# Kernel tuning notes

Hardware: AMD Instinct MI355X
Metric: run time of the kernel (lower is better)

Reference implementation:

```python
import jax, jax.numpy as jnp
import numpy as np

B, L, D_MODEL = 2, 2048, 1024
D_INNER = 2 * D_MODEL          # expand * d_model
D_STATE = 16
D_CONV = 4
DT_RANK = (D_INNER + 15) // 16  # ceil(d_inner/16) = 128


def setup_inputs() -> dict:
    key = jax.random.key(0)
    ks = jax.random.split(key, 9)
    s = 0.02
    x = jax.random.normal(ks[0], (B, L, D_MODEL), jnp.float32)
    in_proj_w = jax.random.normal(ks[1], (2 * D_INNER, D_MODEL), jnp.float32) * s
    conv_w = jax.random.normal(ks[2], (D_INNER, 1, D_CONV), jnp.float32) * s  # depthwise, OIH
    conv_b = jax.random.normal(ks[3], (D_INNER,), jnp.float32) * s
    x_proj_w = jax.random.normal(ks[4], (DT_RANK + 2 * D_STATE, D_INNER), jnp.float32) * s
    dt_proj_w = jax.random.uniform(ks[5], (D_INNER, DT_RANK), jnp.float32, -0.1, 0.1)
    # dt bias: inverse-softplus of dt in [dt_min, dt_max]
    dt = jnp.exp(jax.random.uniform(ks[6], (D_INNER,), jnp.float32)
                 * (np.log(0.1) - np.log(0.001)) + np.log(0.001))
    dt = jnp.clip(dt, 1e-4, None)
    dt_proj_b = dt + jnp.log(-jnp.expm1(-dt))
    A_log = jnp.log(jnp.tile(jnp.arange(1, D_STATE + 1, dtype=jnp.float32), (D_INNER, 1)))
    D = jnp.ones((D_INNER,), jnp.float32)
    out_proj_w = jax.random.normal(ks[7], (D_MODEL, D_INNER), jnp.float32) * s
    return {"x": x, "in_proj_w": in_proj_w, "conv_w": conv_w, "conv_b": conv_b,
            "x_proj_w": x_proj_w, "dt_proj_w": dt_proj_w, "dt_proj_b": dt_proj_b,
            "A_log": A_log, "D": D, "out_proj_w": out_proj_w}


def _s6_forward(x, in_proj_w, conv_w, conv_b, x_proj_w, dt_proj_w, dt_proj_b,
                A_log, D, out_proj_w):
    b, l, _ = x.shape
    d_inner, n_state = A_log.shape
    dt_rank = dt_proj_w.shape[1]
    d_conv = conv_w.shape[-1]

    xz = x @ in_proj_w.T                          # [b, l, 2*d_inner]
    xb, z = jnp.split(xz, 2, axis=-1)

    # causal depthwise conv1d: pad left by d_conv-1, truncate to l
    xc = jnp.swapaxes(xb, 1, 2)                   # [b, d_inner, l]
    xc = jax.lax.conv_general_dilated(
        xc, conv_w, window_strides=(1,), padding=[(d_conv - 1, 0)],
        dimension_numbers=("NCH", "OIH", "NCH"), feature_group_count=d_inner)
    xc = xc + conv_b[None, :, None]
    u = jax.nn.silu(jnp.swapaxes(xc, 1, 2))       # [b, l, d_inner]

    x_dbl = u @ x_proj_w.T                        # [b, l, dt_rank + 2*n_state]
    dt_in, Bs, Cs = jnp.split(x_dbl, [dt_rank, dt_rank + n_state], axis=-1)
    dt = jax.nn.softplus(dt_in @ dt_proj_w.T + dt_proj_b)  # [b, l, d_inner]

    A = -jnp.exp(A_log)                           # [d_inner, n_state]

    def step(h, inp):
        u_t, dt_t, B_t, C_t = inp                 # [b,d], [b,d], [b,n], [b,n]
        dA = jnp.exp(dt_t[:, :, None] * A)        # [b, d, n]
        h = dA * h + (dt_t * u_t)[:, :, None] * B_t[:, None, :]
        y_t = jnp.einsum("bdn,bn->bd", h, C_t)
        return h, y_t

    h0 = jnp.zeros((b, d_inner, n_state), u.dtype)
    xs = (jnp.swapaxes(u, 0, 1), jnp.swapaxes(dt, 0, 1),
          jnp.swapaxes(Bs, 0, 1), jnp.swapaxes(Cs, 0, 1))
    _, ys = jax.lax.scan(step, h0, xs)            # ys: [l, b, d_inner]
    y = jnp.swapaxes(ys, 0, 1) + u * D
    y = y * jax.nn.silu(z)
    return y @ out_proj_w.T                       # [b, l, d_model]


def reference(x, in_proj_w, conv_w, conv_b, x_proj_w, dt_proj_w, dt_proj_b,
              A_log, D, out_proj_w):
    return _s6_forward(x, in_proj_w, conv_w, conv_b, x_proj_w, dt_proj_w,
                       dt_proj_b, A_log, D, out_proj_w)
```

## Files before the change

kernel.cpp:

```cpp
#include <hip/hip_runtime.h>
#include <hip/hip_bf16.h>
#include <math.h>


#define B_ 2
#define L_ 2048
#define DM_ 1024
#define DI_ 2048
#define NS_ 16
#define DTR_ 128
#define XPN_ 160
#define XPP_ 192
#define CH_ 64
#define CL_ 32
#define NCH_ 4096
#define SK_ 8

typedef __attribute__((ext_vector_type(8))) short short8;
typedef __attribute__((ext_vector_type(4))) float f32x4;

__device__ inline unsigned short bfbits(float f) {
    __hip_bfloat16 h = __float2bfloat16(f);
    return *reinterpret_cast<unsigned short*>(&h);
}

__device__ inline void gload16(const void* g, void* l) {
    __builtin_amdgcn_global_load_lds(
        (__attribute__((address_space(1))) const void*)g,
        (__attribute__((address_space(3))) void*)l, 16, 0, 0);
}

__global__ __launch_bounds__(256) void cast_pair(
    const float* __restrict__ s0, unsigned short* __restrict__ d0,
    const float* __restrict__ s1, unsigned short* __restrict__ d1, int nper)
{
    int i = (blockIdx.x * 256 + threadIdx.x) * 4;
    const float* s = s0;
    unsigned short* d = d0;
    if (i >= nper) { s = s1; d = d1; i -= nper; }
    float4 v = *(const float4*)(s + i);
    *(ushort4*)(d + i) = make_ushort4(bfbits(v.x), bfbits(v.y), bfbits(v.z), bfbits(v.w));
}

__global__ __launch_bounds__(256) void cast_flat(
    const float* __restrict__ s, unsigned short* __restrict__ o, int n)
{
    int i = (blockIdx.x * 256 + threadIdx.x) * 4;
    if (i >= n) return;
    float4 v = *(const float4*)(s + i);
    *(ushort4*)(o + i) = make_ushort4(bfbits(v.x), bfbits(v.y), bfbits(v.z), bfbits(v.w));
}

__global__ __launch_bounds__(256) void cast_w(
    const float* __restrict__ xp, unsigned short* __restrict__ WXP,
    const float* __restrict__ dtp, unsigned short* __restrict__ DTP)
{
    int i = (blockIdx.x * 256 + threadIdx.x) * 4;
    const int NW = XPP_ * DI_;
    if (i < NW) {
        int row = i >> 11;
        ushort4 o = make_ushort4(0, 0, 0, 0);
        if (row < XPN_) {
            float4 v = *(const float4*)(xp + i);
            o = make_ushort4(bfbits(v.x), bfbits(v.y), bfbits(v.z), bfbits(v.w));
        }
        *(ushort4*)(WXP + i) = o;
    } else {
        int j = i - NW;
        float4 v = *(const float4*)(dtp + j);
        *(ushort4*)(DTP + j) = make_ushort4(bfbits(v.x), bfbits(v.y), bfbits(v.z), bfbits(v.w));
    }
}

#define GBAR() do { __builtin_amdgcn_s_barrier(); __builtin_amdgcn_sched_barrier(0); } while (0)
#define GWLG() do { asm volatile("s_waitcnt lgkmcnt(0)" ::: "memory"); __builtin_amdgcn_sched_barrier(0); } while (0)
#define GWVM(N) do { asm volatile("s_waitcnt vmcnt(" #N ")" ::: "memory"); __builtin_amdgcn_sched_barrier(0); } while (0)

#define RDA(LA, SWZ, AR) do { _Pragma("unroll") \
    for (int i_ = 0; i_ < 8; ++i_) \
        AR[i_] = *(const short8*)((LA) + aBase + i_ * 2048 + (SWZ)); } while (0)
#define RDB(LB, SWZ, BR) do { _Pragma("unroll") \
    for (int n_ = 0; n_ < 4; ++n_) \
        BR[n_] = *(const short8*)((LB) + bBase + n_ * 2048 + (SWZ)); } while (0)

#define CLUSTER(AR, BR, NF0) do { \
    __builtin_amdgcn_s_setprio(1); \
    _Pragma("unroll") \
    for (int i_ = 0; i_ < 8; ++i_) { \
        acc[i_][NF0]     = __builtin_amdgcn_mfma_f32_16x16x32_bf16(AR[i_], BR[NF0],     acc[i_][NF0],     0, 0, 0); \
        acc[i_][NF0 + 1] = __builtin_amdgcn_mfma_f32_16x16x32_bf16(AR[i_], BR[NF0 + 1], acc[i_][NF0 + 1], 0, 0, 0); \
    } \
    __builtin_amdgcn_s_setprio(0); } while (0)

#define STAGE_A(KT, H, LA) do { \
    const char* gs_ = pA + (long)((H) * 128) * lda2 + (KT) * 128; \
    gload16(gs_ + aoffA,              (LA) + (H) * 16384 + ldsw); \
    gload16(gs_ + aoffA + 64 * (long)lda2, (LA) + (H) * 16384 + 8192 + ldsw); } while (0)
#define STAGE_B(KT, H, LB) do { \
    const char* gs_ = pB + (long)((H) * 128) * ldb2 + (KT) * 128; \
    gload16(gs_ + aoffB,              (LB) + (H) * 16384 + ldsw); \
    gload16(gs_ + aoffB + 64 * (long)ldb2, (LB) + (H) * 16384 + 8192 + ldsw); } while (0)

__global__ __launch_bounds__(512, 2) void gemm_256(
    const unsigned short* __restrict__ A, int lda,
    const unsigned short* __restrict__ B, int ldb,
    float* __restrict__ C, int ldc, int K)
{
    __shared__ __align__(16) char smem[131072];
    char* const L0A = smem;
    char* const L0B = smem + 32768;
    char* const L1A = smem + 65536;
    char* const L1B = smem + 98304;

    const int tid = threadIdx.x;
    const int lane = tid & 63, wave = tid >> 6;
    const int wr = wave >> 2, wc = wave & 3;
    const int m = lane & 15, g = lane >> 4;
    const int row0 = blockIdx.y * 256, col0 = blockIdx.x * 256;

    const int aBase = (wr * 128 + m) * 128;
    const int bBase = (wc * 64 + m) * 128;
    const int swz0 = (g ^ (m & 7)) << 4;
    const int swz1 = ((4 + g) ^ (m & 7)) << 4;

    const int lda2 = lda * 2, ldb2 = ldb * 2;
    const int rowq = tid >> 3;
    const int cswz = ((tid & 7) ^ (rowq & 7)) << 4;
    const long aoffA = (long)rowq * lda2 + cswz;
    const long aoffB = (long)rowq * ldb2 + cswz;
    const char* const pA = (const char*)(A + (long)row0 * lda);
    const char* const pB = (const char*)(B + (long)col0 * ldb);
    const int ldsw = wave << 10;

    f32x4 acc[8][4];
    const f32x4 zero = {0.f, 0.f, 0.f, 0.f};
#pragma unroll
    for (int i = 0; i < 8; ++i)
#pragma unroll
        for (int j = 0; j < 4; ++j) acc[i][j] = zero;

    short8 a0[8], a1[8], b0[4], b1[4];
    const int NT = K >> 6;

    STAGE_B(0, 0, L0B); STAGE_B(0, 1, L0B);
    STAGE_A(0, 0, L0A); STAGE_A(0, 1, L0A);
    STAGE_B(1, 0, L1B); STAGE_B(1, 1, L1B);
    STAGE_A(1, 0, L1A);
    GWVM(6); GBAR();

    for (int t = 0; t < NT - 2; t += 2) {
        RDA(L0A, swz0, a0); RDB(L0B, swz0, b0); RDB(L0B, swz1, b1);
        STAGE_A(t + 1, 1, L1A);
        GBAR(); GWLG();
        CLUSTER(a0, b0, 0);
        GBAR();
        RDA(L0A, swz1, a1);
        STAGE_B(t + 2, 0, L0B);
        GBAR(); GWLG();
        CLUSTER(a0, b0, 2);
        GBAR();
        STAGE_B(t + 2, 1, L0B);
        GBAR();
        CLUSTER(a1, b1, 0);
        GBAR();
        STAGE_A(t + 2, 0, L0A);
        GWVM(6); GBAR();
        CLUSTER(a1, b1, 2);
        GBAR();
        RDA(L1A, swz0, a0); RDB(L1B, swz0, b0); RDB(L1B, swz1, b1);
        STAGE_A(t + 2, 1, L0A);
        GBAR(); GWLG();
        CLUSTER(a0, b0, 0);
        GBAR();
        RDA(L1A, swz1, a1);
        STAGE_B(t + 3, 0, L1B);
        GBAR(); GWLG();
        CLUSTER(a0, b0, 2);
        GBAR();
        STAGE_B(t + 3, 1, L1B);
        GBAR();
        CLUSTER(a1, b1, 0);
        GBAR();
        STAGE_A(t + 3, 0, L1A);
        GWVM(6); GBAR();
        CLUSTER(a1, b1, 2);
        GBAR();
    }

    RDA(L0A, swz0, a0); RDB(L0B, swz0, b0); RDB(L0B, swz1, b1);
    STAGE_A(NT - 1, 1, L1A);
    GBAR(); GWLG();
    CLUSTER(a0, b0, 0);
    GBAR();
    RDA(L0A, swz1, a1);
    GBAR(); GWLG();
    CLUSTER(a0, b0, 2);
    GBAR();
    CLUSTER(a1, b1, 0);
    GBAR();
    GWVM(0); GBAR();
    CLUSTER(a1, b1, 2);
    GBAR();
    RDA(L1A, swz0, a0); RDB(L1B, swz0, b0); RDB(L1B, swz1, b1);
    GWLG();
    CLUSTER(a0, b0, 0);
    RDA(L1A, swz1, a1);
    GWLG();
    CLUSTER(a0, b0, 2);
    CLUSTER(a1, b1, 0);
    CLUSTER(a1, b1, 2);

    const int cr = g << 2;
#pragma unroll
    for (int i = 0; i < 8; ++i) {
        const long gr = row0 + wr * 128 + i * 16 + cr;
#pragma unroll
        for (int nf = 0; nf < 4; ++nf) {
            const int gc = col0 + wc * 64 + nf * 16 + m;
#pragma unroll
            for (int r = 0; r < 4; ++r)
                C[(gr + r) * (long)ldc + gc] = acc[i][nf][r];
        }
    }
}

__global__ __launch_bounds__(256, 2) void gemm_h64(
    const unsigned short* __restrict__ A, int lda,
    const unsigned short* __restrict__ B, int ldb,
    float* __restrict__ C, int ldc, int K)
{
    __shared__ unsigned short sA[128][32];
    __shared__ unsigned short sB[64][32];
    const int tid = threadIdx.x;
    const int lane = tid & 63, wave = tid >> 6;
    const int orig = blockIdx.y * 16 + blockIdx.x;
    const int wgid = (orig & 7) * 64 + (orig >> 3);
    const int row0 = (wgid >> 4) << 7;
    const int col0 = (wgid & 15) << 6;
    const int wr = wave >> 1, wc = wave & 1;
    const int m = lane & 15;
    const int ko = (lane >> 4) << 3;

    f32x4 acc[4][2];
    const f32x4 zero = {0.f, 0.f, 0.f, 0.f};
#pragma unroll
    for (int i = 0; i < 4; ++i)
#pragma unroll
        for (int j = 0; j < 2; ++j) acc[i][j] = zero;

    for (int k0 = 0; k0 < K; k0 += 32) {
#pragma unroll
        for (int c = 0; c < 2; ++c) {
            int idx = tid + (c << 8);
            int r = idx >> 2;
            int col8 = (idx & 3) << 3;
            char* la = (char*)sA + (((c << 8) + (wave << 6)) << 4);
            gload16(A + (long)(row0 + r) * lda + k0 + col8, la);
        }
        {
            int r = tid >> 2;
            int col8 = (tid & 3) << 3;
            char* lb = (char*)sB + ((wave << 6) << 4);
            gload16(B + (long)(col0 + r) * ldb + k0 + col8, lb);
        }
        __syncthreads();

        short8 af[4];
#pragma unroll
        for (int i = 0; i < 4; ++i)
            af[i] = *(const short8*)&sA[(wr << 6) + i * 16 + m][ko];
#pragma unroll
        for (int j = 0; j < 2; ++j) {
            short8 bf = *(const short8*)&sB[(wc << 5) + j * 16 + m][ko];
#pragma unroll
            for (int i = 0; i < 4; ++i)
                acc[i][j] = __builtin_amdgcn_mfma_f32_16x16x32_bf16(af[i], bf, acc[i][j], 0, 0, 0);
        }
        __syncthreads();
    }

    const int cr = (lane >> 4) << 2;
#pragma unroll
    for (int i = 0; i < 4; ++i) {
#pragma unroll
        for (int j = 0; j < 2; ++j) {
            int gr = row0 + (wr << 6) + i * 16 + cr;
            int gc = col0 + (wc << 5) + j * 16 + m;
#pragma unroll
            for (int r = 0; r < 4; ++r)
                C[(long)(gr + r) * ldc + gc] = acc[i][j][r];
        }
    }
}

enum { WE_NONE = 0, WE_SOFTPLUS = 1 };

template <int EPI>
__global__ __launch_bounds__(256) void gemm_w64(
    const unsigned short* __restrict__ A, int lda,
    const unsigned short* __restrict__ B, int ldb,
    float* __restrict__ C, int ldc,
    const float* __restrict__ bias,
    int nstore, int kslice, long partStride)
{
    __shared__ unsigned short sA[64][32];
    __shared__ unsigned short sB[64][32];
    const int tid = threadIdx.x;
    const int lane = tid & 63, wave = tid >> 6;
    const int row0 = blockIdx.y * 64, col0 = blockIdx.x * 64;
    const int m = lane & 15;
    const int ko = (lane >> 4) << 3;
    const int kbeg = blockIdx.z * kslice;
    const int kend = kbeg + kslice;

    const int r = tid >> 2;
    const int c8 = (tid & 3) << 3;
    char* la = (char*)sA + (wave << 10);
    char* lb = (char*)sB + (wave << 10);

    f32x4 acc[4];
    const f32x4 zero = {0.f, 0.f, 0.f, 0.f};
#pragma unroll
    for (int j = 0; j < 4; ++j) acc[j] = zero;

    for (int k0 = kbeg; k0 < kend; k0 += 32) {
        gload16(A + (long)(row0 + r) * lda + k0 + c8, la);
        gload16(B + (long)(col0 + r) * ldb + k0 + c8, lb);
        __syncthreads();

        short8 af = *(const short8*)&sA[(wave << 4) + m][ko];
#pragma unroll
        for (int j = 0; j < 4; ++j) {
            short8 bf = *(const short8*)&sB[j * 16 + m][ko];
            acc[j] = __builtin_amdgcn_mfma_f32_16x16x32_bf16(af, bf, acc[j], 0, 0, 0);
        }
        __syncthreads();
    }

    const int cr = (lane >> 4) << 2;
    const int gr = row0 + (wave << 4) + cr;
    float* Cp = C + (long)blockIdx.z * partStride;
#pragma unroll
    for (int j = 0; j < 4; ++j) {
        int gc = col0 + j * 16 + m;
        if (gc >= nstore) continue;
#pragma unroll
        for (int rr = 0; rr < 4; ++rr) {
            float v = acc[j][rr];
            if (EPI == WE_SOFTPLUS) {
                v += bias[gc];
                v = (v > 20.f) ? v : log1pf(__expf(v));
            }
            Cp[(long)(gr + rr) * ldc + gc] = v;
        }
    }
}

__global__ __launch_bounds__(256) void reduce_part(
    const float* __restrict__ P, float* __restrict__ O,
    unsigned short* __restrict__ O16, int n)
{
    int i = (blockIdx.x * 256 + threadIdx.x) * 4;
    if (i >= n) return;
    float4 s = *(const float4*)(P + i);
#pragma unroll
    for (int k = 1; k < SK_; ++k) {
        float4 v = *(const float4*)(P + (long)k * n + i);
        s.x += v.x; s.y += v.y; s.z += v.z; s.w += v.w;
    }
    *(float4*)(O + i) = s;
    *(ushort4*)(O16 + i) = make_ushort4(bfbits(s.x), bfbits(s.y), bfbits(s.z), bfbits(s.w));
}

__global__ __launch_bounds__(256) void conv_silu(
    const float* __restrict__ xz, const float* __restrict__ w,
    const float* __restrict__ bc, float* __restrict__ U,
    unsigned short* __restrict__ UB)
{
    int e = (blockIdx.x * 256 + threadIdx.x) << 2;
    int d = e & (DI_ - 1);
    int bt = e >> 11;
    int t = bt & (L_ - 1);
    float4 a = *(const float4*)(bc + d);
    float4 w0 = *(const float4*)(w + d * 4);
    float4 w1 = *(const float4*)(w + d * 4 + 4);
    float4 w2 = *(const float4*)(w + d * 4 + 8);
    float4 w3 = *(const float4*)(w + d * 4 + 12);
#pragma unroll
    for (int j = 0; j < 4; ++j) {
        if (t - 3 + j >= 0) {
            float4 xv = *(const float4*)(xz + (long)(bt - 3 + j) * (2 * DI_) + d);
            a.x += ((const float*)&w0)[j] * xv.x;
            a.y += ((const float*)&w1)[j] * xv.y;
            a.z += ((const float*)&w2)[j] * xv.z;
            a.w += ((const float*)&w3)[j] * xv.w;
        }
    }
    float4 u;
    u.x = a.x / (1.f + __expf(-a.x));
    u.y = a.y / (1.f + __expf(-a.y));
    u.z = a.z / (1.f + __expf(-a.z));
    u.w = a.w / (1.f + __expf(-a.w));
    *(float4*)(U + e) = u;
    *(ushort4*)(UB + e) = make_ushort4(bfbits(u.x), bfbits(u.y), bfbits(u.z), bfbits(u.w));
}

__global__ __launch_bounds__(256) void scan_head(
    const float* __restrict__ U, const float* __restrict__ DT,
    const float* __restrict__ XDBL, const float* __restrict__ A_log,
    float* __restrict__ HEND, float* __restrict__ SDT)
{
    const int d = blockIdx.x * 256 + threadIdx.x;
    const int chunk = blockIdx.y;
    const int b = blockIdx.z;
    const int channel = b * DI_ + d;
    const long t0 = (long)b * L_ + chunk * CL_;

    float An[NS_], h[NS_];
#pragma unroll
    for (int n = 0; n < NS_; ++n) {
        An[n] = -__expf(A_log[d * NS_ + n]);
        h[n] = 0.f;
    }
    float sum_dt = 0.f;
    __shared__ float sB[8][NS_];

    for (int tt0 = 0; tt0 < CL_; tt0 += 8) {
        const long bt0 = t0 + tt0;
        if (threadIdx.x < 128) {
            int i = threadIdx.x >> 4, j = threadIdx.x & 15;
            sB[i][j] = XDBL[(bt0 + i) * XPN_ + DTR_ + j];
        }
        __syncthreads();
        float u8[8], dt8[8];
#pragma unroll
        for (int i = 0; i < 8; ++i) u8[i] = U[(bt0 + i) * DI_ + d];
#pragma unroll
        for (int i = 0; i < 8; ++i) dt8[i] = DT[(bt0 + i) * DI_ + d];
#pragma unroll
        for (int i = 0; i < 8; ++i) {
            const float dt = dt8[i];
            sum_dt += dt;
            const float du = dt * u8[i];
#pragma unroll
            for (int n = 0; n < NS_; ++n)
                h[n] = __expf(An[n] * dt) * h[n] + du * sB[i][n];
        }
        __syncthreads();
    }
#pragma unroll
    for (int n = 0; n < NS_; ++n)
        HEND[(chunk * NS_ + n) * NCH_ + channel] = h[n];
    SDT[chunk * NCH_ + channel] = sum_dt;
}

__global__ __launch_bounds__(256) void scan_mid(
    const float* __restrict__ SDT, const float* __restrict__ A_log,
    float* __restrict__ HST)
{
    const int idx = blockIdx.x * 256 + threadIdx.x;
    const int channel = idx & (NCH_ - 1);
    const int n = idx >> 12;
    const int d = channel & (DI_ - 1);
    const float An = -__expf(A_log[d * NS_ + n]);
    float h0 = 0.f;
    for (int c = 0; c < CH_; ++c) {
        const long off = ((long)(c * NS_ + n)) * NCH_ + channel;
        const float he = HST[off];
        HST[off] = h0;
        if (c < CH_ - 1) {
            const float S = SDT[c * NCH_ + channel];
            h0 = __expf(An * S) * h0 + he;
        }
    }
}

__global__ __launch_bounds__(256) void scan_tail(
    const float* __restrict__ U, const float* __restrict__ DT,
    const float* __restrict__ XDBL, const float* __restrict__ A_log,
    const float* __restrict__ Dp, const float* __restrict__ HST,
    float* __restrict__ XZ)
{
    const int d = blockIdx.x * 256 + threadIdx.x;
    const int chunk = blockIdx.y;
    const int b = blockIdx.z;
    const int channel = b * DI_ + d;
    const long t0 = (long)b * L_ + chunk * CL_;
    unsigned short* YOUT = (unsigned short*)XZ;

    float An[NS_], h[NS_];
#pragma unroll
    for (int n = 0; n < NS_; ++n) {
        An[n] = -__expf(A_log[d * NS_ + n]);
        h[n] = HST[(chunk * NS_ + n) * NCH_ + channel];
    }
    const float Dd = Dp[d];
    __shared__ float sB[8][NS_], sC[8][NS_];

    for (int tt0 = 0; tt0 < CL_; tt0 += 8) {
        const long bt0 = t0 + tt0;
        {
            int i = threadIdx.x >> 5, j = threadIdx.x & 31;
            float v = XDBL[(bt0 + i) * XPN_ + DTR_ + j];
            if (j < NS_) sB[i][j] = v; else sC[i][j - NS_] = v;
        }
        __syncthreads();
        float u8[8], dt8[8], z8[8];
        unsigned short y8[8];
#pragma unroll
        for (int i = 0; i < 8; ++i) u8[i] = U[(bt0 + i) * DI_ + d];
#pragma unroll
        for (int i = 0; i < 8; ++i) dt8[i] = DT[(bt0 + i) * DI_ + d];
#pragma unroll
        for (int i = 0; i < 8; ++i) z8[i] = XZ[(bt0 + i) * (2 * DI_) + DI_ + d];
#pragma unroll
        for (int i = 0; i < 8; ++i) {
            const float dt = dt8[i];
            const float du = dt * u8[i];
            float y = 0.f;
#pragma unroll
            for (int n = 0; n < NS_; ++n) {
                h[n] = __expf(An[n] * dt) * h[n] + du * sB[i][n];
                y += h[n] * sC[i][n];
            }
            y += u8[i] * Dd;
            const float z = z8[i];
            y8[i] = bfbits(y * (z / (1.f + __expf(-z))));
        }
#pragma unroll
        for (int i = 0; i < 8; ++i) YOUT[(bt0 + i) * (4 * DI_) + d] = y8[i];
        __syncthreads();
    }
}

extern "C" void kernel_launch(void* const* d_in, const int* in_sizes, int n_in,
                              void* d_out, int out_size, void* d_ws, size_t ws_size,
                              hipStream_t stream)
{
    const float* x        = (const float*)d_in[0];
    const float* in_proj  = (const float*)d_in[1];
    const float* conv_w   = (const float*)d_in[2];
    const float* conv_b   = (const float*)d_in[3];
    const float* x_proj   = (const float*)d_in[4];
    const float* dt_proj  = (const float*)d_in[5];
    const float* dt_projb = (const float*)d_in[6];
    const float* A_log    = (const float*)d_in[7];
    const float* Dp       = (const float*)d_in[8];
    const float* out_proj = (const float*)d_in[9];

    const int M = B_ * L_;
    float* XZ   = (float*)d_ws;
    float* U    = XZ + (size_t)M * 2 * DI_;
    float* XDBL = U + (size_t)M * DI_;
    float* DT   = XDBL + (size_t)M * XPN_;
    float* SDT  = DT + (size_t)M * DI_;
    unsigned short* XDBL16 = (unsigned short*)(SDT + CH_ * NCH_);
    unsigned short* WXP = XDBL16 + (size_t)M * XPN_;
    unsigned short* DTP = WXP + (size_t)XPP_ * DI_;
    float* HEND = (float*)d_out;

    const int NX = M * DM_;
    const int NO = DM_ * DI_;
    unsigned short* XB = (unsigned short*)U;
    unsigned short* WB = (unsigned short*)DT;
    float* PART = DT;
    unsigned short* UB = (unsigned short*)d_out;
    unsigned short* YOUT = (unsigned short*)XZ;
    unsigned short* OB = (unsigned short*)DT;

    cast_pair<<<2 * NX / 1024, 256, 0, stream>>>(x, XB, in_proj, WB, NX);
    cast_w<<<(XPP_ * DI_ + DI_ * DTR_) / 1024, 256, 0, stream>>>(x_proj, WXP, dt_proj, DTP);

    gemm_256<<<dim3(16, 16), 512, 0, stream>>>(
        XB, DM_, WB, DM_, XZ, 2 * DI_, DM_);

    conv_silu<<<(M * DI_) / 1024, 256, 0, stream>>>(XZ, conv_w, conv_b, U, UB);

    gemm_w64<WE_NONE><<<dim3(3, 64, SK_), 256, 0, stream>>>(
        UB, DI_, WXP, DI_, PART, XPN_, nullptr, XPN_, 2048 / SK_, (long)M * XPN_);
    reduce_part<<<(M * XPN_) / 1024, 256, 0, stream>>>(PART, XDBL, XDBL16, M * XPN_);

    gemm_w64<WE_SOFTPLUS><<<dim3(32, 64, 1), 256, 0, stream>>>(
        XDBL16, XPN_, DTP, DTR_, DT, DI_, dt_projb, DI_, DTR_, 0);

    scan_head<<<dim3(8, CH_, B_), 256, 0, stream>>>(U, DT, XDBL, A_log, HEND, SDT);
    scan_mid<<<(NCH_ * NS_) / 256, 256, 0, stream>>>(SDT, A_log, HEND);
    scan_tail<<<dim3(8, CH_, B_), 256, 0, stream>>>(U, DT, XDBL, A_log, Dp, HEND, XZ);

    cast_flat<<<NO / 1024, 256, 0, stream>>>(out_proj, OB, NO);

    gemm_h64<<<dim3(16, 32), 256, 0, stream>>>(
        YOUT, 4 * DI_, OB, DI_, (float*)d_out, DM_, DI_);
}
```

Measured before the change: 327.4 us.

## Store in_proj output and conv activations as bf16 to cut memory traffic

The in_proj GEMM now writes its xz output as bf16 instead of fp32. The conv, scan_head and scan_tail kernels read bf16 x, z and u and widen them in registers, and the separate fp32 U buffer is dropped, so the scans read only the bf16 UB. Buffers are re-laid out so UB sits in the workspace and y overwrites the x half of XZH. This roughly halves the bytes moved by several memory-bound kernels, at the cost of bf16 rounding on intermediates that used to stay fp32, such as z and the scan's u input.

```diff
diff --git a/kernel.cpp b/kernel.cpp
--- a/kernel.cpp
+++ b/kernel.cpp
@@ -24,6 +24,13 @@
     return *reinterpret_cast<unsigned short*>(&h);
 }
 
+__device__ inline float b2f(unsigned short u) {
+    unsigned int x = ((unsigned int)u) << 16;
+    float f;
+    __builtin_memcpy(&f, &x, 4);
+    return f;
+}
+
 __device__ inline void gload16(const void* g, void* l) {
     __builtin_amdgcn_global_load_lds(
         (__attribute__((address_space(1))) const void*)g,
@@ -104,7 +111,7 @@
 __global__ __launch_bounds__(512, 2) void gemm_256(
     const unsigned short* __restrict__ A, int lda,
     const unsigned short* __restrict__ B, int ldb,
-    float* __restrict__ C, int ldc, int K)
+    unsigned short* __restrict__ C, int ldc, int K)
 {
     __shared__ __align__(16) char smem[131072];
     char* const L0A = smem;
@@ -219,7 +226,7 @@
             const int gc = col0 + wc * 64 + nf * 16 + m;
 #pragma unroll
             for (int r = 0; r < 4; ++r)
-                C[(gr + r) * (long)ldc + gc] = acc[i][nf][r];
+                C[(gr + r) * (long)ldc + gc] = bfbits(acc[i][nf][r]);
         }
     }
 }
@@ -373,9 +380,8 @@
 }
 
 __global__ __launch_bounds__(256) void conv_silu(
-    const float* __restrict__ xz, const float* __restrict__ w,
-    const float* __restrict__ bc, float* __restrict__ U,
-    unsigned short* __restrict__ UB)
+    const unsigned short* __restrict__ xzh, const float* __restrict__ w,
+    const float* __restrict__ bc, unsigned short* __restrict__ UB)
 {
     int e = (blockIdx.x * 256 + threadIdx.x) << 2;
     int d = e & (DI_ - 1);
@@ -389,11 +395,11 @@
 #pragma unroll
     for (int j = 0; j < 4; ++j) {
         if (t - 3 + j >= 0) {
-            float4 xv = *(const float4*)(xz + (long)(bt - 3 + j) * (2 * DI_) + d);
-            a.x += ((const float*)&w0)[j] * xv.x;
-            a.y += ((const float*)&w1)[j] * xv.y;
-            a.z += ((const float*)&w2)[j] * xv.z;
-            a.w += ((const float*)&w3)[j] * xv.w;
+            ushort4 xv = *(const ushort4*)(xzh + (long)(bt - 3 + j) * (2 * DI_) + d);
+            a.x += ((const float*)&w0)[j] * b2f(xv.x);
+            a.y += ((const float*)&w1)[j] * b2f(xv.y);
+            a.z += ((const float*)&w2)[j] * b2f(xv.z);
+            a.w += ((const float*)&w3)[j] * b2f(xv.w);
         }
     }
     float4 u;
@@ -401,12 +407,11 @@
     u.y = a.y / (1.f + __expf(-a.y));
     u.z = a.z / (1.f + __expf(-a.z));
     u.w = a.w / (1.f + __expf(-a.w));
-    *(float4*)(U + e) = u;
     *(ushort4*)(UB + e) = make_ushort4(bfbits(u.x), bfbits(u.y), bfbits(u.z), bfbits(u.w));
 }
 
 __global__ __launch_bounds__(256) void scan_head(
-    const float* __restrict__ U, const float* __restrict__ DT,
+    const unsigned short* __restrict__ UB, const float* __restrict__ DT,
     const float* __restrict__ XDBL, const float* __restrict__ A_log,
     float* __restrict__ HEND, float* __restrict__ SDT)
 {
@@ -434,7 +439,7 @@
         __syncthreads();
         float u8[8], dt8[8];
 #pragma unroll
-        for (int i = 0; i < 8; ++i) u8[i] = U[(bt0 + i) * DI_ + d];
+        for (int i = 0; i < 8; ++i) u8[i] = b2f(UB[(bt0 + i) * DI_ + d]);
 #pragma unroll
         for (int i = 0; i < 8; ++i) dt8[i] = DT[(bt0 + i) * DI_ + d];
 #pragma unroll
@@ -476,17 +481,16 @@
 }
 
 __global__ __launch_bounds__(256) void scan_tail(
-    const float* __restrict__ U, const float* __restrict__ DT,
+    const unsigned short* __restrict__ UB, const float* __restrict__ DT,
     const float* __restrict__ XDBL, const float* __restrict__ A_log,
     const float* __restrict__ Dp, const float* __restrict__ HST,
-    float* __restrict__ XZ)
+    unsigned short* __restrict__ XZH)
 {
     const int d = blockIdx.x * 256 + threadIdx.x;
     const int chunk = blockIdx.y;
     const int b = blockIdx.z;
     const int channel = b * DI_ + d;
     const long t0 = (long)b * L_ + chunk * CL_;
-    unsigned short* YOUT = (unsigned short*)XZ;
 
     float An[NS_], h[NS_];
 #pragma unroll
@@ -508,11 +512,11 @@
         float u8[8], dt8[8], z8[8];
         unsigned short y8[8];
 #pragma unroll
-        for (int i = 0; i < 8; ++i) u8[i] = U[(bt0 + i) * DI_ + d];
+        for (int i = 0; i < 8; ++i) u8[i] = b2f(UB[(bt0 + i) * DI_ + d]);
 #pragma unroll
         for (int i = 0; i < 8; ++i) dt8[i] = DT[(bt0 + i) * DI_ + d];
 #pragma unroll
-        for (int i = 0; i < 8; ++i) z8[i] = XZ[(bt0 + i) * (2 * DI_) + DI_ + d];
+        for (int i = 0; i < 8; ++i) z8[i] = b2f(XZH[(bt0 + i) * (2 * DI_) + DI_ + d]);
 #pragma unroll
         for (int i = 0; i < 8; ++i) {
             const float dt = dt8[i];
@@ -528,7 +532,7 @@
             y8[i] = bfbits(y * (z / (1.f + __expf(-z))));
         }
 #pragma unroll
-        for (int i = 0; i < 8; ++i) YOUT[(bt0 + i) * (4 * DI_) + d] = y8[i];
+        for (int i = 0; i < 8; ++i) XZH[(bt0 + i) * (2 * DI_) + d] = y8[i];
         __syncthreads();
     }
 }
@@ -549,11 +553,11 @@
     const float* out_proj = (const float*)d_in[9];
 
     const int M = B_ * L_;
-    float* XZ   = (float*)d_ws;
-    float* U    = XZ + (size_t)M * 2 * DI_;
-    float* XDBL = U + (size_t)M * DI_;
-    float* DT   = XDBL + (size_t)M * XPN_;
-    float* SDT  = DT + (size_t)M * DI_;
+    unsigned short* XZH = (unsigned short*)d_ws;
+    float* Uslot = (float*)d_ws + (size_t)M * 2 * DI_;
+    float* XDBL  = Uslot + (size_t)M * DI_;
+    float* DT    = XDBL + (size_t)M * XPN_;
+    float* SDT   = DT + (size_t)M * DI_;
     unsigned short* XDBL16 = (unsigned short*)(SDT + CH_ * NCH_);
     unsigned short* WXP = XDBL16 + (size_t)M * XPN_;
     unsigned short* DTP = WXP + (size_t)XPP_ * DI_;
@@ -561,20 +565,19 @@
 
     const int NX = M * DM_;
     const int NO = DM_ * DI_;
-    unsigned short* XB = (unsigned short*)U;
+    unsigned short* UB = (unsigned short*)Uslot;
+    unsigned short* XB = UB;
     unsigned short* WB = (unsigned short*)DT;
     float* PART = DT;
-    unsigned short* UB = (unsigned short*)d_out;
-    unsigned short* YOUT = (unsigned short*)XZ;
     unsigned short* OB = (unsigned short*)DT;
 
     cast_pair<<<2 * NX / 1024, 256, 0, stream>>>(x, XB, in_proj, WB, NX);
     cast_w<<<(XPP_ * DI_ + DI_ * DTR_) / 1024, 256, 0, stream>>>(x_proj, WXP, dt_proj, DTP);
 
     gemm_256<<<dim3(16, 16), 512, 0, stream>>>(
-        XB, DM_, WB, DM_, XZ, 2 * DI_, DM_);
-
-    conv_silu<<<(M * DI_) / 1024, 256, 0, stream>>>(XZ, conv_w, conv_b, U, UB);
+        XB, DM_, WB, DM_, XZH, 2 * DI_, DM_);
+
+    conv_silu<<<(M * DI_) / 1024, 256, 0, stream>>>(XZH, conv_w, conv_b, UB);
 
     gemm_w64<WE_NONE><<<dim3(3, 64, SK_), 256, 0, stream>>>(
         UB, DI_, WXP, DI_, PART, XPN_, nullptr, XPN_, 2048 / SK_, (long)M * XPN_);
@@ -583,12 +586,12 @@
     gemm_w64<WE_SOFTPLUS><<<dim3(32, 64, 1), 256, 0, stream>>>(
         XDBL16, XPN_, DTP, DTR_, DT, DI_, dt_projb, DI_, DTR_, 0);
 
-    scan_head<<<dim3(8, CH_, B_), 256, 0, stream>>>(U, DT, XDBL, A_log, HEND, SDT);
+    scan_head<<<dim3(8, CH_, B_), 256, 0, stream>>>(UB, DT, XDBL, A_log, HEND, SDT);
     scan_mid<<<(NCH_ * NS_) / 256, 256, 0, stream>>>(SDT, A_log, HEND);
-    scan_tail<<<dim3(8, CH_, B_), 256, 0, stream>>>(U, DT, XDBL, A_log, Dp, HEND, XZ);
+    scan_tail<<<dim3(8, CH_, B_), 256, 0, stream>>>(UB, DT, XDBL, A_log, Dp, HEND, XZH);
 
     cast_flat<<<NO / 1024, 256, 0, stream>>>(out_proj, OB, NO);
 
     gemm_h64<<<dim3(16, 32), 256, 0, stream>>>(
-        YOUT, 4 * DI_, OB, DI_, (float*)d_out, DM_, DI_);
-}
+        XZH, 2 * DI_, OB, DI_, (float*)d_out, DM_, DI_);
+}
```

Result: no change. 322.2 us (-1.6%).
